# Performance work log

Measured on AMD Instinct MI355X. Metric: run time of the kernel, lower is better.

The kernel has to match this reference:

```python
import jax, jax.numpy as jnp
import numpy as np

BIG = 1e30
B, Hh, Ww, DM = 8, 64, 64, 128
DI = 2 * DM          # d_inner
RR = -(-DM // 16)    # dt_rank = ceil(DM/16)
HID = 512


def _ln(x, g, b, eps):
    mu = jnp.mean(x, -1, keepdims=True)
    var = jnp.mean((x - mu) ** 2, -1, keepdims=True)
    return (x - mu) * jax.lax.rsqrt(var + eps) * g + b


def _silu(x):
    return x * jax.nn.sigmoid(x)


def _grid_weights(f):
    # f: [D,H,W]; MST edge weights exp(-cosine_sim) on 4-connected grid, BIG = invalid
    def cos(a, b):
        num = jnp.sum(a * b, 0)
        den = jnp.maximum(jnp.linalg.norm(a, axis=0) * jnp.linalg.norm(b, axis=0), 1e-8)
        return num / den
    wr = jnp.pad(jnp.exp(-cos(f[:, :, :-1], f[:, :, 1:])), ((0, 0), (0, 1)), constant_values=BIG).reshape(-1)
    wd = jnp.pad(jnp.exp(-cos(f[:, :-1, :], f[:, 1:, :])), ((0, 1), (0, 0)), constant_values=BIG).reshape(-1)
    return wr, wd


def _mst(wr, wd, H, W):
    # Prim's minimum spanning tree on HxW grid. Addition order is a valid
    # topological order (parent precedes child), equivalent to the BFS sort
    # for the order-invariant tree-scan aggregation.
    L = H * W

    def body(t, st):
        dist, par, intree, order = st
        v = jnp.argmin(jnp.where(intree, BIG, dist)).astype(jnp.int32)
        intree = intree.at[v].set(True)
        order = order.at[t].set(v)
        r, c = v // W, v % W
        for u, valid, w in (
            (v + 1, c < W - 1, wr[v]),
            (v - 1, c > 0, wr[jnp.clip(v - 1, 0, L - 1)]),
            (v + W, r < H - 1, wd[v]),
            (v - W, r > 0, wd[jnp.clip(v - W, 0, L - 1)]),
        ):
            uc = jnp.clip(u, 0, L - 1)
            better = valid & (~intree[uc]) & (w < dist[uc])
            dist = dist.at[uc].set(jnp.where(better, w, dist[uc]))
            par = par.at[uc].set(jnp.where(better, v, par[uc]))
        return dist, par, intree, order

    st0 = (jnp.full((L,), BIG, jnp.float32).at[0].set(-1.0),
           jnp.zeros((L,), jnp.int32),
           jnp.zeros((L,), bool),
           jnp.zeros((L,), jnp.int32))
    _, par, _, order = jax.lax.fori_loop(0, L, body, st0)
    return order, par


def _tree_scan(feat, ew, order, par):
    # feat, ew: [D,L]. Two-pass tree filter: out[i] = sum_j prod_{e in path(i,j)} w_e * f[j]
    vs = order[1:]
    ps = par[vs]

    def up_step(up, vp):
        v, p = vp
        return up.at[:, p].add(ew[:, v] * up[:, v]), None

    up, _ = jax.lax.scan(up_step, feat, (vs[::-1], ps[::-1]))
    root = order[0]
    out0 = jnp.zeros_like(up).at[:, root].set(up[:, root])

    def down_step(out, vp):
        v, p = vp
        w = ew[:, v]
        return out.at[:, v].set(up[:, v] + w * (out[:, p] - w * up[:, v])), None

    out, _ = jax.lax.scan(down_step, out0, (vs, ps))
    return out


def reference(x, ln1_g, ln1_b, ln2_g, ln2_b, w_in, conv_w, x_weight, dt_weight,
              dt_bias, a_logs, ds, hn_g, hn_b, on_g, on_b, w_out,
              mlp_w1, mlp_b1, mlp_w2, mlp_b2):
    Bb, H, W, _ = x.shape
    L = H * W
    # --- TreeScan branch ---
    h = _ln(x, ln1_g, ln1_b, 1e-6)
    xc, z = jnp.split(h @ w_in.T, 2, -1)
    z = _silu(z)
    xc = jnp.transpose(xc, (0, 3, 1, 2))                      # [B,Di,H,W]
    xc = _silu(jax.lax.conv_general_dilated(
        xc, conv_w, (1, 1), ((1, 1), (1, 1)),
        dimension_numbers=('NCHW', 'OIHW', 'NCHW'),
        feature_group_count=xc.shape[1]))
    Di = xc.shape[1]
    xs = xc.reshape(Bb, Di, L)
    R = dt_weight.shape[2]
    x_dbl = jnp.einsum('bdl,cd->bcl', xs, x_weight[0])        # [B,R+2,L]
    dts, Bs, Cs = x_dbl[:, :R], x_dbl[:, R:R + 1], x_dbl[:, R + 1:]
    dts = jnp.einsum('brl,dr->bdl', dts, dt_weight[0])
    dts = jax.nn.softplus(dts + dt_bias.reshape(-1)[None, :, None])
    As = -jnp.exp(a_logs.reshape(-1).astype(jnp.float32))     # N=1
    deltaA = jnp.exp(dts * As[None, :, None])                 # per-channel edge weights
    feat_in = dts * Bs * xs                                   # deltaB * x (K=N=1)
    # MST + topological sort under no-grad (matches torch.no_grad())
    f4t = jax.lax.stop_gradient(xs).reshape(Bb, Di, H, W)
    wr, wd = jax.vmap(_grid_weights)(f4t)
    order, par = jax.vmap(lambda a, b: _mst(a, b, H, W))(wr, wd)
    feat_out = jax.vmap(_tree_scan)(feat_in, deltaA, order, par)  # [B,Di,L]
    ho = _ln(jnp.swapaxes(feat_out, 1, 2), hn_g, hn_b, 1e-5)      # h_norm
    y = jnp.swapaxes(ho * jnp.swapaxes(Cs, 1, 2), 1, 2)           # multiply by Cs (N=1)
    y = y + ds[None, :, None] * xs                                # D skip
    y = _ln(jnp.swapaxes(y, 1, 2), on_g, on_b, 1e-5).reshape(Bb, H, W, Di)
    scan_out = (y * z) @ w_out.T
    # --- residual + MLP ---
    x1 = x + scan_out
    h2 = _ln(x1, ln2_g, ln2_b, 1e-6)
    mlp = jax.nn.gelu(h2 @ mlp_w1.T + mlp_b1) @ mlp_w2.T + mlp_b2
    return x1 + mlp


def setup_inputs():
    key = jax.random.key(0)
    ks = jax.random.split(key, 12)

    def rn(k, shape, s):
        return jax.random.normal(k, shape, jnp.float32) * s

    dt = jnp.exp(jax.random.uniform(ks[10], (DI,)) * (np.log(0.1) - np.log(0.001)) + np.log(0.001))
    dt_bias = (dt + jnp.log(-jnp.expm1(-dt)))[None]  # inverse-softplus init
    return {
        'x': rn(ks[0], (B, Hh, Ww, DM), 1.0),
        'ln1_g': jnp.ones((DM,)), 'ln1_b': jnp.zeros((DM,)),
        'ln2_g': jnp.ones((DM,)), 'ln2_b': jnp.zeros((DM,)),
        'w_in': rn(ks[1], (2 * DI, DM), DM ** -0.5),
        'conv_w': rn(ks[2], (DI, 1, 3, 3), 1.0 / 3.0),
        'x_weight': rn(ks[3], (1, RR + 2, DI), DI ** -0.5),
        'dt_weight': rn(ks[4], (1, DI, RR), RR ** -0.5),
        'dt_bias': dt_bias,
        'a_logs': jnp.zeros((DI, 1)),
        'ds': jnp.ones((DI,)),
        'hn_g': jnp.ones((DI,)), 'hn_b': jnp.zeros((DI,)),
        'on_g': jnp.ones((DI,)), 'on_b': jnp.zeros((DI,)),
        'w_out': rn(ks[5], (DM, DI), DI ** -0.5),
        'mlp_w1': rn(ks[6], (HID, DM), DM ** -0.5),
        'mlp_b1': jnp.zeros((HID,)),
        'mlp_w2': rn(ks[7], (DM, HID), HID ** -0.5),
        'mlp_b2': jnp.zeros((DM,)),
    }
```

## Files before the change

kernel.cpp:

```cpp
#include <hip/hip_runtime.h>
#include <hip/hip_bf16.h>
#include <cstdint>

#define BIGF 1e30f
constexpr int LB   = 4096;
constexpr int NB   = 8;
constexpr int MROWS = NB * LB;
constexpr int LSP  = 4104;

__device__ __forceinline__ float warp_sum(float v) {
#pragma unroll
  for (int off = 32; off; off >>= 1) v += __shfl_xor(v, off);
  return v;
}

template<int EPI>
__global__ __launch_bounds__(256) void gemm_kernel(
    const float* __restrict__ A, const float* __restrict__ W,
    float* __restrict__ C, float* __restrict__ C2,
    const float* __restrict__ bias, const float* __restrict__ addsrc,
    int M, int N, int K) {
  __shared__ float As[32][68];
  __shared__ float Bs[32][68];
  int t = threadIdx.x;
  int tx = t & 15, ty = t >> 4;
  int bm = blockIdx.y * 64, bn = blockIdx.x * 64;
  float acc[4][4] = {};
  for (int k0 = 0; k0 < K; k0 += 32) {
#pragma unroll
    for (int hh = 0; hh < 2; ++hh) {
      int q = t + hh * 256;
      int r = q >> 3, kc = q & 7;
      float4 a4 = reinterpret_cast<const float4*>(A + (size_t)(bm + r) * K + k0)[kc];
      float4 b4 = reinterpret_cast<const float4*>(W + (size_t)(bn + r) * K + k0)[kc];
      As[kc * 4 + 0][r] = a4.x; As[kc * 4 + 1][r] = a4.y;
      As[kc * 4 + 2][r] = a4.z; As[kc * 4 + 3][r] = a4.w;
      Bs[kc * 4 + 0][r] = b4.x; Bs[kc * 4 + 1][r] = b4.y;
      Bs[kc * 4 + 2][r] = b4.z; Bs[kc * 4 + 3][r] = b4.w;
    }
    __syncthreads();
#pragma unroll
    for (int kk = 0; kk < 32; ++kk) {
      float4 av = *reinterpret_cast<const float4*>(&As[kk][ty * 4]);
      float4 bv = *reinterpret_cast<const float4*>(&Bs[kk][tx * 4]);
      float aa[4] = {av.x, av.y, av.z, av.w};
      float bbv[4] = {bv.x, bv.y, bv.z, bv.w};
#pragma unroll
      for (int i = 0; i < 4; ++i)
#pragma unroll
        for (int j = 0; j < 4; ++j) acc[i][j] += aa[i] * bbv[j];
    }
    __syncthreads();
  }
#pragma unroll
  for (int i = 0; i < 4; ++i) {
    int m = bm + ty * 4 + i;
#pragma unroll
    for (int j = 0; j < 4; ++j) {
      int n = bn + tx * 4 + j;
      float v = acc[i][j];
      if (EPI == 2) {
        C[(size_t)m * N + n] = v + addsrc[(size_t)m * N + n];
      } else if (EPI == 4) {
        C[(size_t)m * N + n] = v + bias[n] + addsrc[(size_t)m * N + n];
      }
    }
  }
}

template<int EPI>
__global__ __launch_bounds__(256) void gemm128ln_kernel(
    const float* __restrict__ A, const float* __restrict__ W,
    float* __restrict__ C, float* __restrict__ C2,
    const float* __restrict__ bias, const float* __restrict__ lng,
    const float* __restrict__ lnb, int M, int N, int K) {
  __shared__ float As[32][132];
  __shared__ float Bs[32][132];
  __shared__ float mu_s[128], rs_s[128], g_s[128], b_s[128];
  int t = threadIdx.x;
  int tx = t & 15, ty = t >> 4;
  int bm = blockIdx.y * 128, bn = blockIdx.x * 128;
  {
    int r = t >> 1, hf = t & 1;
    const float4* row = reinterpret_cast<const float4*>(A + (size_t)(bm + r) * K + hf * 64);
    float s = 0.f;
#pragma unroll
    for (int i = 0; i < 16; ++i) { float4 v = row[i]; s += v.x + v.y + v.z + v.w; }
    s += __shfl_xor(s, 1);
    float mu = s * (1.0f / 128.0f);
    float sq = 0.f;
#pragma unroll
    for (int i = 0; i < 16; ++i) {
      float4 v = row[i];
      float d0 = v.x - mu, d1 = v.y - mu, d2 = v.z - mu, d3 = v.w - mu;
      sq += d0 * d0 + d1 * d1 + d2 * d2 + d3 * d3;
    }
    sq += __shfl_xor(sq, 1);
    if (hf == 0) {
      mu_s[r] = mu;
      rs_s[r] = 1.0f / sqrtf(sq * (1.0f / 128.0f) + 1e-6f);
    }
    if (t < 128) { g_s[t] = lng[t]; b_s[t] = lnb[t]; }
  }
  __syncthreads();
  float acc[8][8] = {};
  for (int k0 = 0; k0 < K; k0 += 32) {
#pragma unroll
    for (int hh = 0; hh < 4; ++hh) {
      int q = t + hh * 256;
      int r = q >> 3, kc = q & 7;
      float4 a4 = *reinterpret_cast<const float4*>(A + (size_t)(bm + r) * K + k0 + kc * 4);
      float4 b4 = *reinterpret_cast<const float4*>(W + (size_t)(bn + r) * K + k0 + kc * 4);
      float mu = mu_s[r], rs = rs_s[r];
      int c0 = k0 + kc * 4;
      As[kc * 4 + 0][r] = (a4.x - mu) * rs * g_s[c0]     + b_s[c0];
      As[kc * 4 + 1][r] = (a4.y - mu) * rs * g_s[c0 + 1] + b_s[c0 + 1];
      As[kc * 4 + 2][r] = (a4.z - mu) * rs * g_s[c0 + 2] + b_s[c0 + 2];
      As[kc * 4 + 3][r] = (a4.w - mu) * rs * g_s[c0 + 3] + b_s[c0 + 3];
      Bs[kc * 4 + 0][r] = b4.x; Bs[kc * 4 + 1][r] = b4.y;
      Bs[kc * 4 + 2][r] = b4.z; Bs[kc * 4 + 3][r] = b4.w;
    }
    __syncthreads();
#pragma unroll
    for (int kk = 0; kk < 32; ++kk) {
      float4 a0 = *reinterpret_cast<const float4*>(&As[kk][ty * 4]);
      float4 a1 = *reinterpret_cast<const float4*>(&As[kk][64 + ty * 4]);
      float4 b0 = *reinterpret_cast<const float4*>(&Bs[kk][tx * 4]);
      float4 b1 = *reinterpret_cast<const float4*>(&Bs[kk][64 + tx * 4]);
      float aa[8] = {a0.x, a0.y, a0.z, a0.w, a1.x, a1.y, a1.z, a1.w};
      float bb2[8] = {b0.x, b0.y, b0.z, b0.w, b1.x, b1.y, b1.z, b1.w};
#pragma unroll
      for (int i = 0; i < 8; ++i)
#pragma unroll
        for (int j = 0; j < 8; ++j) acc[i][j] += aa[i] * bb2[j];
    }
    __syncthreads();
  }
#pragma unroll
  for (int i = 0; i < 8; ++i) {
    int m = bm + (i >> 2) * 64 + ty * 4 + (i & 3);
#pragma unroll
    for (int j = 0; j < 8; ++j) {
      int n = bn + (j >> 2) * 64 + tx * 4 + (j & 3);
      float v = acc[i][j];
      if (EPI == 1) {
        if (n < 256) C[(size_t)m * 256 + n] = v;
        else C2[(size_t)m * 256 + (n - 256)] = v / (1.0f + __expf(-v));
      } else if (EPI == 3) {
        float u = v + bias[n];
        float xg = 1.5957691216057308f * (u + 0.044715f * u * u * u);
        C[(size_t)m * N + n] = u / (1.0f + __expf(-xg));
      }
    }
  }
}

__global__ __launch_bounds__(256) void convfeat_kernel(
    const float* __restrict__ xcpre, const float* __restrict__ cw,
    const float* __restrict__ xw, const float* __restrict__ dtw,
    const float* __restrict__ dtb, const float* __restrict__ alogs,
    float* __restrict__ xs, float* __restrict__ dAt, float* __restrict__ featt,
    float* __restrict__ Cs, float* __restrict__ ssq) {
  int m = blockIdx.x;
  int d = threadIdx.x;
  int l = m & (LB - 1), b = m >> 12;
  int r = l >> 6, c = l & 63;
  float acc = 0.f;
#pragma unroll
  for (int ky = 0; ky < 3; ++ky) {
    int rr = r + ky - 1;
    if (rr < 0 || rr > 63) continue;
#pragma unroll
    for (int kx = 0; kx < 3; ++kx) {
      int cc = c + kx - 1;
      if (cc < 0 || cc > 63) continue;
      int ml = (b << 12) + (rr << 6) + cc;
      acc += xcpre[(size_t)ml * 256 + d] * cw[d * 9 + ky * 3 + kx];
    }
  }
  float xv = acc / (1.0f + __expf(-acc));
  xs[(size_t)m * 256 + d] = xv;
  float p[11];
#pragma unroll
  for (int i = 0; i < 10; ++i) p[i] = xv * xw[i * 256 + d];
  p[10] = xv * xv;
  __shared__ float sm[4][11];
#pragma unroll
  for (int i = 0; i < 11; ++i) p[i] = warp_sum(p[i]);
  int wv = d >> 6;
  if ((d & 63) == 0) {
    for (int i = 0; i < 11; ++i) sm[wv][i] = p[i];
  }
  __syncthreads();
  float red[11];
#pragma unroll
  for (int i = 0; i < 11; ++i) red[i] = sm[0][i] + sm[1][i] + sm[2][i] + sm[3][i];
  float xdt = dtb[d];
#pragma unroll
  for (int rr2 = 0; rr2 < 8; ++rr2) xdt += red[rr2] * dtw[d * 8 + rr2];
  float sp = fmaxf(xdt, 0.f) + __logf(1.0f + __expf(-fabsf(xdt)));
  float As_ = -__expf(alogs[d]);
  size_t tidx = ((size_t)(b * 64 + (d >> 2)) * 4096 + l) * 4 + (d & 3);
  dAt[tidx]   = __expf(sp * As_);
  featt[tidx] = sp * red[8] * xv;
  if (d == 0) { Cs[m] = red[9]; ssq[m] = red[10]; }
}

__global__ __launch_bounds__(256) void gridw_kernel(
    const float* __restrict__ xs, const float* __restrict__ ssq,
    float* __restrict__ wrg, float* __restrict__ wdg) {
  int m = blockIdx.x, d = threadIdx.x;
  int l = m & (LB - 1);
  int r = l >> 6, c = l & 63;
  float a = xs[(size_t)m * 256 + d];
  float br = (c < 63) ? xs[(size_t)(m + 1) * 256 + d] : 0.f;
  float bd = (r < 63) ? xs[(size_t)(m + 64) * 256 + d] : 0.f;
  float s1 = warp_sum(a * br);
  float s2 = warp_sum(a * bd);
  __shared__ float sm[4][2];
  int wv = d >> 6;
  if ((d & 63) == 0) { sm[wv][0] = s1; sm[wv][1] = s2; }
  __syncthreads();
  if (d == 0) {
    float dotr = sm[0][0] + sm[1][0] + sm[2][0] + sm[3][0];
    float dotd = sm[0][1] + sm[1][1] + sm[2][1] + sm[3][1];
    float na = sqrtf(ssq[m]);
    float wrv = BIGF, wdv = BIGF;
    if (c < 63) { float den = fmaxf(na * sqrtf(ssq[m + 1]), 1e-8f);  wrv = expf(-(dotr / den)); }
    if (r < 63) { float den = fmaxf(na * sqrtf(ssq[m + 64]), 1e-8f); wdv = expf(-(dotd / den)); }
    wrg[m] = wrv; wdg[m] = wdv;
  }
}

__global__ __launch_bounds__(1024) void mst_kernel(
    const float* __restrict__ wr_g, const float* __restrict__ wd_g,
    unsigned int* __restrict__ topo_g, int* __restrict__ levs_g) {
  __shared__ int pool[24592];
  __shared__ unsigned char flagR[4096];
  __shared__ unsigned char flagD[4096];
  __shared__ int ncomp_s;
  __shared__ int wred[16];
  int b = blockIdx.x, tid = threadIdx.x;
  float* wrs = (float*)pool;
  float* wds = (float*)(pool + 4096);
  int* comp = pool + 8192;
  int* lnk  = pool + 12288;
  unsigned int* bestw = (unsigned int*)(pool + 16384);
  int* beste = pool + 20480;
  const float* wrb = wr_g + b * 4096;
  const float* wdb = wd_g + b * 4096;
  for (int k = 0; k < 4; ++k) {
    int i = tid + k * 1024;
    wrs[i] = wrb[i]; wds[i] = wdb[i];
    comp[i] = i; flagR[i] = 0; flagD[i] = 0;
  }
  __syncthreads();
  for (int phase = 0; phase < 13; ++phase) {
    for (int k = 0; k < 4; ++k) {
      int c = tid + k * 1024;
      bestw[c] = 0xFFFFFFFFu; beste[c] = 0x7FFFFFFF; lnk[c] = c;
    }
    if (tid == 0) ncomp_s = 0;
    __syncthreads();
    for (int k = 0; k < 8; ++k) {
      int e = tid + k * 1024;
      int v = e & 4095;
      bool isR = e < 4096;
      int c = v & 63, r = v >> 6;
      bool valid = isR ? (c < 63) : (r < 63);
      if (valid) {
        int u = isR ? v + 1 : v + 64;
        int ca = comp[v], cb = comp[u];
        if (ca != cb) {
          unsigned wbits = __float_as_uint(isR ? wrs[v] : wds[v]);
          atomicMin(&bestw[ca], wbits);
          atomicMin(&bestw[cb], wbits);
        }
      }
    }
    __syncthreads();
    for (int k = 0; k < 8; ++k) {
      int e = tid + k * 1024;
      int v = e & 4095;
      bool isR = e < 4096;
      int c = v & 63, r = v >> 6;
      bool valid = isR ? (c < 63) : (r < 63);
      if (valid) {
        int u = isR ? v + 1 : v + 64;
        int ca = comp[v], cb = comp[u];
        if (ca != cb) {
          unsigned wbits = __float_as_uint(isR ? wrs[v] : wds[v]);
          if (wbits == bestw[ca]) atomicMin(&beste[ca], e);
          if (wbits == bestw[cb]) atomicMin(&beste[cb], e);
        }
      }
    }
    __syncthreads();
    for (int k = 0; k < 4; ++k) {
      int cc = tid + k * 1024;
      int e = beste[cc];
      if (e != 0x7FFFFFFF) {
        int v = e & 4095;
        bool isR = e < 4096;
        int u = isR ? v + 1 : v + 64;
        if (isR) flagR[v] = 1; else flagD[v] = 1;
        int ca = comp[v], cb = comp[u];
        lnk[cc] = (ca == cc) ? cb : ca;
      }
    }
    __syncthreads();
    for (int k = 0; k < 4; ++k) {
      int cc = tid + k * 1024;
      int l = lnk[cc];
      if (l != cc && lnk[l] == cc && cc < l) lnk[cc] = cc;
    }
    __syncthreads();
    for (int it = 0; it < 12; ++it) {
      for (int k = 0; k < 4; ++k) {
        int cc = tid + k * 1024;
        lnk[cc] = lnk[lnk[cc]];
      }
      __syncthreads();
    }
    for (int k = 0; k < 4; ++k) {
      int i = tid + k * 1024;
      comp[i] = lnk[comp[i]];
      if (comp[i] == i) atomicAdd(&ncomp_s, 1);
    }
    __syncthreads();
    if (ncomp_s <= 1) break;
    __syncthreads();
  }
  unsigned short* nxt = (unsigned short*)pool;
  short*          dsv = (short*)(pool + 8200);
  int* par = pool + 16400;
  int* dep = pool + 20496;
  const int NIL = 16384;
  unsigned short rn[16];
  int rd[16];
  int validm = 0;
  for (int k = 0; k < 4; ++k) { int i = tid + k * 1024; par[i] = 0; dep[i] = 0; }
#pragma unroll
  for (int k = 0; k < 16; ++k) {
    int a = tid + k * 1024;
    int u = a >> 2, d = a & 3;
    int c = u & 63, r = u >> 6;
    int mu = 0;
    if (r > 0  && flagD[u - 64]) mu |= 1;
    if (c > 0  && flagR[u - 1])  mu |= 2;
    if (c < 63 && flagR[u])      mu |= 4;
    if (r < 63 && flagD[u])      mu |= 8;
    unsigned short nx = NIL; short dv = 0;
    if (mu & (1 << d)) {
      validm |= 1 << k;
      int v = u + ((d == 0) ? -64 : (d == 1) ? -1 : (d == 2) ? 1 : 64);
      int cv = v & 63, rv = v >> 6;
      int mv = 0;
      if (rv > 0  && flagD[v - 64]) mv |= 1;
      if (cv > 0  && flagR[v - 1])  mv |= 2;
      if (cv < 63 && flagR[v])      mv |= 4;
      if (rv < 63 && flagD[v])      mv |= 8;
      int din = 3 - d;
      int hi = mv >> (din + 1);
      int dn = hi ? (din + __ffs(hi)) : (__ffs(mv) - 1);
      int nxv = v * 4 + dn;
      int m0 = (flagR[0] ? 4 : 0) | (flagD[0] ? 8 : 0);
      int a0 = __ffs(m0) - 1;
      if (v == 0 && nxv == a0) nxv = NIL;
      nx = (unsigned short)nxv;
      dv = 1;
    }
    nxt[a] = nx; dsv[a] = dv;
    rn[k] = nx; rd[k] = dv;
  }
  if (tid == 0) { nxt[NIL] = NIL; dsv[NIL] = 0; }
  __syncthreads();
#pragma unroll 1
  for (int it = 0; it < 13; ++it) {
    unsigned short nn[16]; short nd[16];
#pragma unroll
    for (int k = 0; k < 16; ++k) { nn[k] = nxt[rn[k]]; nd[k] = dsv[rn[k]]; }
    __syncthreads();
#pragma unroll
    for (int k = 0; k < 16; ++k) {
      int a = tid + k * 1024;
      rd[k] += nd[k];
      rn[k] = nn[k];
      nxt[a] = rn[k]; dsv[a] = (short)rd[k];
    }
    __syncthreads();
  }
#pragma unroll
  for (int k = 0; k < 16; ++k) if (validm & (1 << k)) {
    int a = tid + k * 1024;
    int u = a >> 2, d = a & 3;
    int v = u + ((d == 0) ? -64 : (d == 1) ? -1 : (d == 2) ? 1 : 64);
    int rb = v * 4 + (3 - d);
    if (rd[k] > (int)dsv[rb]) par[v] = u;
  }
  __syncthreads();
#pragma unroll
  for (int k = 0; k < 16; ++k) {
    int a = tid + k * 1024;
    int u = a >> 2, d = a & 3;
    unsigned short nx = NIL; short dv = 0;
    if (validm & (1 << k)) {
      int v = u + ((d == 0) ? -64 : (d == 1) ? -1 : (d == 2) ? 1 : 64);
      int cv = v & 63, rv = v >> 6;
      int mv = 0;
      if (rv > 0  && flagD[v - 64]) mv |= 1;
      if (cv > 0  && flagR[v - 1])  mv |= 2;
      if (cv < 63 && flagR[v])      mv |= 4;
      if (rv < 63 && flagD[v])      mv |= 8;
      int din = 3 - d;
      int hi = mv >> (din + 1);
      int dn = hi ? (din + __ffs(hi)) : (__ffs(mv) - 1);
      int nxv = v * 4 + dn;
      int m0 = (flagR[0] ? 4 : 0) | (flagD[0] ? 8 : 0);
      int a0 = __ffs(m0) - 1;
      if (v == 0 && nxv == a0) nxv = NIL;
      nx = (unsigned short)nxv;
      dv = (par[v] == u) ? (short)1 : (short)-1;
    }
    nxt[a] = nx; dsv[a] = dv;
    rn[k] = nx; rd[k] = dv;
  }
  __syncthreads();
#pragma unroll 1
  for (int it = 0; it < 13; ++it) {
    unsigned short nn[16]; short nd[16];
#pragma unroll
    for (int k = 0; k < 16; ++k) { nn[k] = nxt[rn[k]]; nd[k] = dsv[rn[k]]; }
    __syncthreads();
#pragma unroll
    for (int k = 0; k < 16; ++k) {
      int a = tid + k * 1024;
      rd[k] += nd[k];
      rn[k] = nn[k];
      nxt[a] = rn[k]; dsv[a] = (short)rd[k];
    }
    __syncthreads();
  }
#pragma unroll
  for (int k = 0; k < 16; ++k) if (validm & (1 << k)) {
    int a = tid + k * 1024;
    int u = a >> 2, d = a & 3;
    int v = u + ((d == 0) ? -64 : (d == 1) ? -1 : (d == 2) ? 1 : 64);
    if (par[v] == u) dep[v] = 1 - rd[k];
  }
  __syncthreads();
  int md = 0;
  for (int k = 0; k < 4; ++k) md = max(md, dep[tid + k * 1024]);
#pragma unroll
  for (int off = 32; off; off >>= 1) md = max(md, __shfl_xor(md, off));
  if ((tid & 63) == 0) wred[tid >> 6] = md;
  __syncthreads();
  if (tid == 0) {
    int m = 0;
    for (int i = 0; i < 16; ++i) m = max(m, wred[i]);
    wred[0] = m;
  }
  __syncthreads();
  int maxd = wred[0];
  __syncthreads();
  int* cnt  = pool;
  int* offs = pool + 4096;
  for (int k = 0; k < 4; ++k) cnt[tid + k * 1024] = 0;
  __syncthreads();
  for (int k = 0; k < 4; ++k) atomicAdd(&cnt[dep[tid + k * 1024]], 1);
  __syncthreads();
  int base4 = tid * 4;
  int c0 = cnt[base4], c1 = cnt[base4 + 1], c2 = cnt[base4 + 2], c3 = cnt[base4 + 3];
  int tsum = c0 + c1 + c2 + c3;
  int lane = tid & 63, wid = tid >> 6;
  int iv = tsum;
  for (int off = 1; off < 64; off <<= 1) {
    int n = __shfl_up(iv, off);
    if (lane >= off) iv += n;
  }
  if (lane == 63) wred[wid] = iv;
  __syncthreads();
  if (tid == 0) {
    int acc = 0;
    for (int i = 0; i < 16; ++i) { int t = wred[i]; wred[i] = acc; acc += t; }
  }
  __syncthreads();
  int excl = iv - tsum + wred[wid];
  offs[base4]     = excl;
  offs[base4 + 1] = excl + c0;
  offs[base4 + 2] = excl + c0 + c1;
  offs[base4 + 3] = excl + c0 + c1 + c2;
  __syncthreads();
  for (int idx = tid; idx <= maxd; idx += 1024) levs_g[b * LSP + idx] = offs[idx];
  if (tid == 0) {
    levs_g[b * LSP + maxd + 1] = 4096;
    levs_g[b * LSP + 4098] = maxd + 1;
  }
  __syncthreads();
  for (int k = 0; k < 4; ++k) {
    int v2 = tid + k * 1024;
    int pos = atomicAdd(&offs[dep[v2]], 1);
    int c = v2 & 63, r = v2 >> 6;
    unsigned msk = 0;
    if (r > 0  && par[v2 - 64] == v2) msk |= 1;
    if (c > 0  && par[v2 - 1]  == v2) msk |= 2;
    if (c < 63 && par[v2 + 1]  == v2) msk |= 4;
    if (r < 63 && par[v2 + 64] == v2) msk |= 8;
    topo_g[b * 4096 + pos] =
        (unsigned)v2 | (msk << 12) | ((unsigned)par[v2] << 16);
  }
}

__global__ __launch_bounds__(64) void scan_kernel(
    float* __restrict__ buft, const float* __restrict__ ewt,
    const unsigned int* __restrict__ topo_g, const int* __restrict__ levs_g) {
  __shared__ float acc[16384];
  __shared__ unsigned short lvs[4104];
  int bid = blockIdx.x;
  int b = bid >> 6, cg = bid & 63;
  int lane = threadIdx.x;
  int ch = lane & 3, slot = lane >> 2;
  int nlev = levs_g[b * LSP + 4098];
  size_t fbase = (size_t)(b * 64 + cg) * 16384;
  const float4* bt4 = reinterpret_cast<const float4*>(buft + fbase);
  const float*  ewf = ewt + fbase;
  const float4* et4 = reinterpret_cast<const float4*>(ewf);
  const unsigned int* tp = topo_g + b * 4096;
  float4* acc4 = reinterpret_cast<float4*>(acc);
  float wsum = 0.f;
  for (int n = lane; n < 4096; n += 64) {
    acc4[n] = bt4[n];
    float4 ev = et4[n];
    wsum += ev.x + ev.y + ev.z + ev.w;
  }
  asm volatile("" :: "v"(wsum));
  for (int i = lane; i <= nlev; i += 64) lvs[i] = (unsigned short)levs_g[b * LSP + i];
  __syncthreads();
  if (nlev > 1) {
    int lev0 = nlev - 1;
    int jA = lvs[lev0] + slot, eA = lvs[lev0 + 1];
    unsigned tA = tp[jA < 4096 ? jA : 4095];
    float elA = ewf[(tA & 4095) * 4 + ch];
    int jB = 0, eB = 0; unsigned tB = 0; float elB = 0.f;
    if (lev0 - 1 >= 1) {
      jB = lvs[lev0 - 1] + slot; eB = lvs[lev0];
      tB = tp[jB < 4096 ? jB : 4095];
      elB = ewf[(tB & 4095) * 4 + ch];
    }
    int jC = 0, eC = 0; unsigned tC = 0;
    if (lev0 - 2 >= 1) {
      jC = lvs[lev0 - 2] + slot; eC = lvs[lev0 - 1];
      tC = tp[jC < 4096 ? jC : 4095];
    }
    for (int lev = lev0; lev >= 1; --lev) {
      float elC = 0.f;
      if (lev - 2 >= 1) elC = ewf[(tC & 4095) * 4 + ch];
      int jD = 0, eD = 0; unsigned tD = 0;
      if (lev - 3 >= 1) {
        jD = lvs[lev - 3] + slot; eD = lvs[lev - 2];
        tD = tp[jD < 4096 ? jD : 4095];
      }
      if (jA < eA) {
        int vA = tA & 4095, pA = (tA >> 16) & 4095;
        float a = acc[vA * 4 + ch];
        atomicAdd(&acc[pA * 4 + ch], elA * a);
        for (int j = jA + 16; j < eA; j += 16) {
          unsigned t = tp[j];
          int v = t & 4095, p = (t >> 16) & 4095;
          float e = ewf[v * 4 + ch];
          float av = acc[v * 4 + ch];
          atomicAdd(&acc[p * 4 + ch], e * av);
        }
      }
      __builtin_amdgcn_wave_barrier();
      jA = jB; eA = eB; tA = tB; elA = elB;
      jB = jC; eB = eC; tB = tC; elB = elC;
      jC = jD; eC = eD; tC = tD;
    }
  }
  __builtin_amdgcn_wave_barrier();
  if (nlev > 1) {
    int jA = lvs[1] + slot, eA = lvs[2];
    unsigned tA = tp[jA < 4096 ? jA : 4095];
    float elA = ewf[(tA & 4095) * 4 + ch];
    int jB = 0, eB = 0; unsigned tB = 0; float elB = 0.f;
    if (2 < nlev) {
      jB = lvs[2] + slot; eB = lvs[3];
      tB = tp[jB < 4096 ? jB : 4095];
      elB = ewf[(tB & 4095) * 4 + ch];
    }
    int jC = 0, eC = 0; unsigned tC = 0;
    if (3 < nlev) {
      jC = lvs[3] + slot; eC = lvs[4];
      tC = tp[jC < 4096 ? jC : 4095];
    }
    for (int lev = 1; lev < nlev; ++lev) {
      float elC = 0.f;
      if (lev + 2 < nlev) elC = ewf[(tC & 4095) * 4 + ch];
      int jD = 0, eD = 0; unsigned tD = 0;
      if (lev + 3 < nlev) {
        jD = lvs[lev + 3] + slot; eD = lvs[lev + 4];
        tD = tp[jD < 4096 ? jD : 4095];
      }
      if (jA < eA) {
        int vA = tA & 4095, pA = (tA >> 16) & 4095;
        float uv = acc[vA * 4 + ch];
        float pb = acc[pA * 4 + ch];
        acc[vA * 4 + ch] = uv + elA * (pb - elA * uv);
        for (int j = jA + 16; j < eA; j += 16) {
          unsigned t = tp[j];
          int v = t & 4095, p = (t >> 16) & 4095;
          float e = ewf[v * 4 + ch];
          float uvv = acc[v * 4 + ch];
          float pbv = acc[p * 4 + ch];
          acc[v * 4 + ch] = uvv + e * (pbv - e * uvv);
        }
      }
      __builtin_amdgcn_wave_barrier();
      jA = jB; eA = eB; tA = tB; elA = elB;
      jB = jC; eB = eC; tB = tC; elB = elC;
      jC = jD; eC = eD; tC = tD;
    }
  }
  __syncthreads();
  float4* bw4 = reinterpret_cast<float4*>(buft + fbase);
  for (int n = lane; n < 4096; n += 64) bw4[n] = acc4[n];
}

__global__ __launch_bounds__(256) void post_kernel(
    const float* __restrict__ buft, const float* __restrict__ Cs,
    const float* __restrict__ xs, const float* __restrict__ ds,
    const float* __restrict__ hng, const float* __restrict__ hnb,
    const float* __restrict__ ong, const float* __restrict__ onb,
    float* __restrict__ zya) {
  int w = threadIdx.x >> 6, lane = threadIdx.x & 63;
  int m = blockIdx.x * 4 + w;
  int b = m >> 12, l = m & (LB - 1);
  float4 fo = *reinterpret_cast<const float4*>(
      buft + ((size_t)(b * 64 + lane) * 4096 + l) * 4);
  float mu = warp_sum(fo.x + fo.y + fo.z + fo.w) * (1.f / 256.f);
  float4 dv = make_float4(fo.x - mu, fo.y - mu, fo.z - mu, fo.w - mu);
  float var = warp_sum(dv.x * dv.x + dv.y * dv.y + dv.z * dv.z + dv.w * dv.w) * (1.f / 256.f);
  float rs = 1.0f / sqrtf(var + 1e-5f);
  float4 hg = reinterpret_cast<const float4*>(hng)[lane];
  float4 hb = reinterpret_cast<const float4*>(hnb)[lane];
  float csv = Cs[m];
  float4 dsv4 = reinterpret_cast<const float4*>(ds)[lane];
  float4 xv = reinterpret_cast<const float4*>(xs + (size_t)m * 256)[lane];
  float y0 = (dv.x * rs * hg.x + hb.x) * csv + dsv4.x * xv.x;
  float y1 = (dv.y * rs * hg.y + hb.y) * csv + dsv4.y * xv.y;
  float y2_ = (dv.z * rs * hg.z + hb.z) * csv + dsv4.z * xv.z;
  float y3 = (dv.w * rs * hg.w + hb.w) * csv + dsv4.w * xv.w;
  float mu2 = warp_sum(y0 + y1 + y2_ + y3) * (1.f / 256.f);
  float d0 = y0 - mu2, d1 = y1 - mu2, d2 = y2_ - mu2, d3 = y3 - mu2;
  float var2 = warp_sum(d0 * d0 + d1 * d1 + d2 * d2 + d3 * d3) * (1.f / 256.f);
  float rs2 = 1.0f / sqrtf(var2 + 1e-5f);
  float4 og = reinterpret_cast<const float4*>(ong)[lane];
  float4 ob = reinterpret_cast<const float4*>(onb)[lane];
  float4* zp = reinterpret_cast<float4*>(zya + (size_t)m * 256) + lane;
  float4 zv = *zp;
  zv.x = (d0 * rs2 * og.x + ob.x) * zv.x;
  zv.y = (d1 * rs2 * og.y + ob.y) * zv.y;
  zv.z = (d2 * rs2 * og.z + ob.z) * zv.z;
  zv.w = (d3 * rs2 * og.w + ob.w) * zv.w;
  *zp = zv;
}

extern "C" void kernel_launch(void* const* d_in, const int* in_sizes, int n_in,
                              void* d_out, int out_size, void* d_ws, size_t ws_size,
                              hipStream_t stream) {
  (void)in_sizes; (void)n_in; (void)out_size; (void)ws_size;
  const float* x      = (const float*)d_in[0];
  const float* ln1g   = (const float*)d_in[1];
  const float* ln1b   = (const float*)d_in[2];
  const float* ln2g   = (const float*)d_in[3];
  const float* ln2b   = (const float*)d_in[4];
  const float* w_in   = (const float*)d_in[5];
  const float* conv_w = (const float*)d_in[6];
  const float* xw     = (const float*)d_in[7];
  const float* dtw    = (const float*)d_in[8];
  const float* dtb    = (const float*)d_in[9];
  const float* alogs  = (const float*)d_in[10];
  const float* dsv    = (const float*)d_in[11];
  const float* hng    = (const float*)d_in[12];
  const float* hnb    = (const float*)d_in[13];
  const float* ong    = (const float*)d_in[14];
  const float* onb    = (const float*)d_in[15];
  const float* w_out  = (const float*)d_in[16];
  const float* mw1    = (const float*)d_in[17];
  const float* mb1    = (const float*)d_in[18];
  const float* mw2    = (const float*)d_in[19];
  const float* mb2    = (const float*)d_in[20];

  char* ws = (char*)d_ws;
  float* x1   = (float*)(ws + 0);
  float* z    = (float*)(ws + 16777216);
  float* xcp  = (float*)(ws + 50331648);
  float* xs   = (float*)(ws + 83886080);
  float* dAt  = (float*)(ws + 117440512);
  float* featt= (float*)(ws + 150994944);
  float* Cs   = (float*)(ws + 184549376);
  float* ssq  = (float*)(ws + 184680448);
  float* wr   = (float*)(ws + 184811520);
  float* wd   = (float*)(ws + 184942592);
  unsigned int* topo32 = (unsigned int*)(ws + 185073664);
  int*   levs = (int*)(ws + 185335808);
  float* midg = xs;

  gemm128ln_kernel<1><<<dim3(4, 256), 256, 0, stream>>>(x, w_in, xcp, z, nullptr,
                                                        ln1g, ln1b, MROWS, 512, 128);
  convfeat_kernel<<<MROWS, 256, 0, stream>>>(xcp, conv_w, xw, dtw, dtb, alogs,
                                             xs, dAt, featt, Cs, ssq);
  gridw_kernel<<<MROWS, 256, 0, stream>>>(xs, ssq, wr, wd);
  mst_kernel<<<NB, 1024, 0, stream>>>(wr, wd, topo32, levs);
  scan_kernel<<<512, 64, 0, stream>>>(featt, dAt, topo32, levs);
  post_kernel<<<MROWS / 4, 256, 0, stream>>>(featt, Cs, xs, dsv, hng, hnb, ong, onb, z);
  gemm_kernel<2><<<dim3(2, 512), 256, 0, stream>>>(z, w_out, x1, nullptr, nullptr, x,
                                                   MROWS, 128, 256);
  gemm128ln_kernel<3><<<dim3(4, 256), 256, 0, stream>>>(x1, mw1, midg, nullptr, mb1,
                                                        ln2g, ln2b, MROWS, 512, 128);
  gemm_kernel<4><<<dim3(2, 512), 256, 0, stream>>>(midg, mw2, (float*)d_out, nullptr,
                                                   mb2, x1, MROWS, 128, 512);
}
```

Before: 833.5 us.

## Map one wavefront per pixel in conv/gridw kernels and trim MST pointer-jumping

```diff
diff --git a/kernel.cpp b/kernel.cpp
--- a/kernel.cpp
+++ b/kernel.cpp
@@ -161,11 +161,17 @@
     const float* __restrict__ dtb, const float* __restrict__ alogs,
     float* __restrict__ xs, float* __restrict__ dAt, float* __restrict__ featt,
     float* __restrict__ Cs, float* __restrict__ ssq) {
-  int m = blockIdx.x;
-  int d = threadIdx.x;
+  __shared__ float cws[9 * 256];
+  int t = threadIdx.x;
+#pragma unroll
+  for (int k = 0; k < 9; ++k) cws[k * 256 + t] = cw[t * 9 + k];
+  __syncthreads();
+  int w = t >> 6, lane = t & 63;
+  int m = blockIdx.x * 4 + w;
   int l = m & (LB - 1), b = m >> 12;
   int r = l >> 6, c = l & 63;
-  float acc = 0.f;
+  const float4* xc4 = reinterpret_cast<const float4*>(xcpre);
+  float ax = 0.f, ay = 0.f, az = 0.f, aw = 0.f;
 #pragma unroll
   for (int ky = 0; ky < 3; ++ky) {
     int rr = r + ky - 1;
@@ -175,59 +181,71 @@
       int cc = c + kx - 1;
       if (cc < 0 || cc > 63) continue;
       int ml = (b << 12) + (rr << 6) + cc;
-      acc += xcpre[(size_t)ml * 256 + d] * cw[d * 9 + ky * 3 + kx];
-    }
-  }
-  float xv = acc / (1.0f + __expf(-acc));
-  xs[(size_t)m * 256 + d] = xv;
-  float p[11];
-#pragma unroll
-  for (int i = 0; i < 10; ++i) p[i] = xv * xw[i * 256 + d];
-  p[10] = xv * xv;
-  __shared__ float sm[4][11];
-#pragma unroll
-  for (int i = 0; i < 11; ++i) p[i] = warp_sum(p[i]);
-  int wv = d >> 6;
-  if ((d & 63) == 0) {
-    for (int i = 0; i < 11; ++i) sm[wv][i] = p[i];
-  }
-  __syncthreads();
+      float4 v = xc4[(size_t)ml * 64 + lane];
+      float4 wv = *reinterpret_cast<const float4*>(&cws[(ky * 3 + kx) * 256 + lane * 4]);
+      ax += v.x * wv.x; ay += v.y * wv.y; az += v.z * wv.z; aw += v.w * wv.w;
+    }
+  }
+  float4 xv;
+  xv.x = ax / (1.0f + __expf(-ax));
+  xv.y = ay / (1.0f + __expf(-ay));
+  xv.z = az / (1.0f + __expf(-az));
+  xv.w = aw / (1.0f + __expf(-aw));
+  reinterpret_cast<float4*>(xs)[(size_t)m * 64 + lane] = xv;
   float red[11];
 #pragma unroll
-  for (int i = 0; i < 11; ++i) red[i] = sm[0][i] + sm[1][i] + sm[2][i] + sm[3][i];
-  float xdt = dtb[d];
-#pragma unroll
-  for (int rr2 = 0; rr2 < 8; ++rr2) xdt += red[rr2] * dtw[d * 8 + rr2];
-  float sp = fmaxf(xdt, 0.f) + __logf(1.0f + __expf(-fabsf(xdt)));
-  float As_ = -__expf(alogs[d]);
-  size_t tidx = ((size_t)(b * 64 + (d >> 2)) * 4096 + l) * 4 + (d & 3);
-  dAt[tidx]   = __expf(sp * As_);
-  featt[tidx] = sp * red[8] * xv;
-  if (d == 0) { Cs[m] = red[9]; ssq[m] = red[10]; }
+  for (int i = 0; i < 10; ++i) {
+    float4 wv = reinterpret_cast<const float4*>(xw)[i * 64 + lane];
+    red[i] = warp_sum(xv.x * wv.x + xv.y * wv.y + xv.z * wv.z + xv.w * wv.w);
+  }
+  red[10] = warp_sum(xv.x * xv.x + xv.y * xv.y + xv.z * xv.z + xv.w * xv.w);
+  float4 dtb4 = reinterpret_cast<const float4*>(dtb)[lane];
+  float4 al4  = reinterpret_cast<const float4*>(alogs)[lane];
+  float xdt[4] = {dtb4.x, dtb4.y, dtb4.z, dtb4.w};
+#pragma unroll
+  for (int j = 0; j < 4; ++j) {
+    int d = lane * 4 + j;
+    float4 w0 = *reinterpret_cast<const float4*>(dtw + d * 8);
+    float4 w1 = *reinterpret_cast<const float4*>(dtw + d * 8 + 4);
+    xdt[j] += red[0] * w0.x + red[1] * w0.y + red[2] * w0.z + red[3] * w0.w
+            + red[4] * w1.x + red[5] * w1.y + red[6] * w1.z + red[7] * w1.w;
+  }
+  float alv[4] = {al4.x, al4.y, al4.z, al4.w};
+  float4 dA4, ft4;
+  float* dAp = &dA4.x;
+  float* ftp = &ft4.x;
+#pragma unroll
+  for (int j = 0; j < 4; ++j) {
+    float sp = fmaxf(xdt[j], 0.f) + __logf(1.0f + __expf(-fabsf(xdt[j])));
+    float As_ = -__expf(alv[j]);
+    dAp[j] = __expf(sp * As_);
+    float xvj = (j == 0) ? xv.x : (j == 1) ? xv.y : (j == 2) ? xv.z : xv.w;
+    ftp[j] = sp * red[8] * xvj;
+  }
+  size_t tb = (size_t)(b * 64 + lane) * 4096 + l;
+  reinterpret_cast<float4*>(dAt)[tb]   = dA4;
+  reinterpret_cast<float4*>(featt)[tb] = ft4;
+  if (lane == 0) { Cs[m] = red[9]; ssq[m] = red[10]; }
 }
 
 __global__ __launch_bounds__(256) void gridw_kernel(
     const float* __restrict__ xs, const float* __restrict__ ssq,
     float* __restrict__ wrg, float* __restrict__ wdg) {
-  int m = blockIdx.x, d = threadIdx.x;
+  int w = threadIdx.x >> 6, lane = threadIdx.x & 63;
+  int m = blockIdx.x * 4 + w;
   int l = m & (LB - 1);
   int r = l >> 6, c = l & 63;
-  float a = xs[(size_t)m * 256 + d];
-  float br = (c < 63) ? xs[(size_t)(m + 1) * 256 + d] : 0.f;
-  float bd = (r < 63) ? xs[(size_t)(m + 64) * 256 + d] : 0.f;
-  float s1 = warp_sum(a * br);
-  float s2 = warp_sum(a * bd);
-  __shared__ float sm[4][2];
-  int wv = d >> 6;
-  if ((d & 63) == 0) { sm[wv][0] = s1; sm[wv][1] = s2; }
-  __syncthreads();
-  if (d == 0) {
-    float dotr = sm[0][0] + sm[1][0] + sm[2][0] + sm[3][0];
-    float dotd = sm[0][1] + sm[1][1] + sm[2][1] + sm[3][1];
+  const float4* xs4 = reinterpret_cast<const float4*>(xs);
+  float4 a = xs4[(size_t)m * 64 + lane];
+  float4 br = (c < 63) ? xs4[(size_t)(m + 1) * 64 + lane] : make_float4(0, 0, 0, 0);
+  float4 bd = (r < 63) ? xs4[(size_t)(m + 64) * 64 + lane] : make_float4(0, 0, 0, 0);
+  float s1 = warp_sum(a.x * br.x + a.y * br.y + a.z * br.z + a.w * br.w);
+  float s2 = warp_sum(a.x * bd.x + a.y * bd.y + a.z * bd.z + a.w * bd.w);
+  if (lane == 0) {
     float na = sqrtf(ssq[m]);
     float wrv = BIGF, wdv = BIGF;
-    if (c < 63) { float den = fmaxf(na * sqrtf(ssq[m + 1]), 1e-8f);  wrv = expf(-(dotr / den)); }
-    if (r < 63) { float den = fmaxf(na * sqrtf(ssq[m + 64]), 1e-8f); wdv = expf(-(dotd / den)); }
+    if (c < 63) { float den = fmaxf(na * sqrtf(ssq[m + 1]), 1e-8f);  wrv = expf(-(s1 / den)); }
+    if (r < 63) { float den = fmaxf(na * sqrtf(ssq[m + 64]), 1e-8f); wdv = expf(-(s2 / den)); }
     wrg[m] = wrv; wdg[m] = wdv;
   }
 }
@@ -315,7 +333,8 @@
       if (l != cc && lnk[l] == cc && cc < l) lnk[cc] = cc;
     }
     __syncthreads();
-    for (int it = 0; it < 12; ++it) {
+    int iters = 12 - phase; if (iters < 3) iters = 3;
+    for (int it = 0; it < iters; ++it) {
       for (int k = 0; k < 4; ++k) {
         int cc = tid + k * 1024;
         lnk[cc] = lnk[lnk[cc]];
@@ -709,9 +728,9 @@
 
   gemm128ln_kernel<1><<<dim3(4, 256), 256, 0, stream>>>(x, w_in, xcp, z, nullptr,
                                                         ln1g, ln1b, MROWS, 512, 128);
-  convfeat_kernel<<<MROWS, 256, 0, stream>>>(xcp, conv_w, xw, dtw, dtb, alogs,
-                                             xs, dAt, featt, Cs, ssq);
-  gridw_kernel<<<MROWS, 256, 0, stream>>>(xs, ssq, wr, wd);
+  convfeat_kernel<<<MROWS / 4, 256, 0, stream>>>(xcp, conv_w, xw, dtw, dtb, alogs,
+                                                 xs, dAt, featt, Cs, ssq);
+  gridw_kernel<<<MROWS / 4, 256, 0, stream>>>(xs, ssq, wr, wd);
   mst_kernel<<<NB, 1024, 0, stream>>>(wr, wd, topo32, levs);
   scan_kernel<<<512, 64, 0, stream>>>(featt, dAt, topo32, levs);
   post_kernel<<<MROWS / 4, 256, 0, stream>>>(featt, Cs, xs, dsv, hng, hnb, ong, onb, z);
```

New measurement: 782.5 us, median of 2. 6.1% less time.
